# Kernel tuning notes

Measured on AMD Instinct MI355X. Metric: run time of the kernel, lower is better.

## Reference

```python
import jax, jax.numpy as jnp
import numpy as np

D = 768        # TEXT_DIM
N = 50         # seq len (h,w = 1,50 in source)
HEADS = 8
LABEL_SIZE = 50
B = 512
EPS_COS = 1e-8
EPS_LN = 1e-5


def _egce(x, w):
    # EGCE source not provided in repo snippet; implemented as ECA-style efficient
    # gated channel excitation: GAP over HW -> 1D conv (k=3) over channels -> sigmoid gate.
    gap = x.mean(axis=(2, 3))                      # [b, c]
    p = jnp.pad(gap, ((0, 0), (1, 1)))
    att = jax.nn.sigmoid(w[0] * p[:, :-2] + w[1] * p[:, 1:-1] + w[2] * p[:, 2:])
    return x * att[:, :, None, None]


def _lstm(x, Wih, Whh, bih, bhh):
    # PyTorch single-layer batch_first LSTM, gate order i,f,g,o, zero init state.
    b, n, d = x.shape
    xg = jnp.einsum('bnd,gd->bng', x, Wih) + bih + bhh   # [b, n, 4d]
    def step(carry, xt):
        h, c = carry
        g = xt + h @ Whh.T
        i, f, gg, o = jnp.split(g, 4, axis=-1)
        c = jax.nn.sigmoid(f) * c + jax.nn.sigmoid(i) * jnp.tanh(gg)
        h = jax.nn.sigmoid(o) * jnp.tanh(c)
        return (h, c), h
    h0 = jnp.zeros((b, d), x.dtype)
    _, ys = jax.lax.scan(step, (h0, h0), jnp.swapaxes(xg, 0, 1))
    return jnp.swapaxes(ys, 0, 1)


def _cross_attn(q_in, kv_in, qW, qb, kW, kb, vW, vb):
    b, n, d = q_in.shape
    dh = d // HEADS
    q = (q_in @ qW.T + qb).reshape(b, n, HEADS, dh).transpose(0, 2, 1, 3)
    k = (kv_in @ kW.T + kb).reshape(b, -1, HEADS, dh).transpose(0, 2, 1, 3)
    v = (kv_in @ vW.T + vb).reshape(b, -1, HEADS, dh).transpose(0, 2, 1, 3)
    attn = jax.nn.softmax(jnp.einsum('bhqd,bhkd->bhqk', q, k) * dh ** -0.5, axis=-1)
    # NOTE: faithful to source: einsum('bhqk,bhvd->bhqd') sums k and v INDEPENDENTLY
    out = jnp.einsum('bhqk,bhvd->bhqd', attn, v)
    return out.transpose(0, 2, 1, 3).reshape(b, n, d)


def _ln(x, g, b):
    m = x.mean(-1, keepdims=True)
    v = ((x - m) ** 2).mean(-1, keepdims=True)
    return (x - m) * jax.lax.rsqrt(v + EPS_LN) * g + b


def setup_inputs() -> dict:
    key = jax.random.key(0)
    ks = jax.random.split(key, 24)
    s = 0.02
    def w(k, shape):
        return jax.random.normal(k, shape, jnp.float32) * s
    vis_emb = w(ks[0], (LABEL_SIZE + 1, D)).at[LABEL_SIZE].set(0.0)
    ac_emb = w(ks[1], (LABEL_SIZE + 1, D)).at[LABEL_SIZE].set(0.0)
    inp = {
        'text_embedding': jax.random.normal(ks[2], (B, N, D), jnp.float32),
        'visual_ids': jax.random.randint(ks[3], (B, N), 0, LABEL_SIZE),
        'acoustic_ids': jax.random.randint(ks[4], (B, N), 0, LABEL_SIZE),
        'vis_emb': vis_emb,
        'ac_emb': ac_emb,
        'egce_w': w(ks[5], (3,)) + 0.3,
        'lstm_Wih': w(ks[6], (4 * D, D)),
        'lstm_Whh': w(ks[7], (4 * D, D)),
        'lstm_bih': jnp.zeros((4 * D,), jnp.float32),
        'lstm_bhh': jnp.zeros((4 * D,), jnp.float32),
        'ln_g': jnp.ones((D,), jnp.float32),
        'ln_b': jnp.zeros((D,), jnp.float32),
        'concat_W': w(ks[8], (D, 3 * D)),
        'concat_b': jnp.zeros((D,), jnp.float32),
        'hybrid_W': w(ks[9], (D, 3 * D)),
        'hybrid_b': jnp.zeros((D,), jnp.float32),
        # stacked cross-attention params, index 0 = cross_att_t, 1 = cross_att_a, 2 = cross_att_v
        'ca_qW': w(ks[10], (3, D, D)), 'ca_qb': w(ks[11], (3, D)),
        'ca_kW': w(ks[12], (3, D, D)), 'ca_kb': w(ks[13], (3, D)),
        'ca_vW': w(ks[14], (3, D, D)), 'ca_vb': w(ks[15], (3, D)),
    }
    return inp


def _forward(text_embedding, vis_emb, ac_emb, egce_w, lstm_Wih, lstm_Whh,
             lstm_bih, lstm_bhh, ln_g, ln_b, concat_W, concat_b, hybrid_W,
             hybrid_b, ca_qW, ca_qb, ca_kW, ca_kb, ca_vW, ca_vb,
             visual_ids, acoustic_ids):
    b, n, c = text_embedding.shape
    visual_ = jax.nn.relu(vis_emb[visual_ids])
    acoustic_ = ac_emb[acoustic_ids]
    # faithful reshape (NOT transpose) [b,n,c] -> [b,c,1,n] -> egce -> [b,n,c]
    text = _egce(text_embedding.reshape(b, c, 1, n), egce_w).reshape(b, n, c)
    visual_ = _egce(visual_.reshape(b, c, 1, n), egce_w).reshape(b, n, c)
    acoustic_ = _egce(acoustic_.reshape(b, c, 1, n), egce_w).reshape(b, n, c)

    # ---- AFI (vectorized over batch via masks instead of Python loop) ----
    def cos(x, y):
        xm, ym = x.mean(1), y.mean(1)
        nx = jnp.maximum(jnp.sqrt((xm * xm).sum(-1)), EPS_COS)
        ny = jnp.maximum(jnp.sqrt((ym * ym).sum(-1)), EPS_COS)
        return (xm * ym).sum(-1) / (nx * ny)
    rtv, rta, rva = cos(text, visual_), cos(text, acoustic_), cos(visual_, acoustic_)
    delta = (rtv + rta + rva) / 3.0
    joint = (rtv + rta + rva) / 3.0   # identical to delta in source
    cat = jnp.concatenate([text, visual_, acoustic_], axis=-1)  # [b,n,3d]
    f_concat = cat @ concat_W.T + concat_b
    f_hybrid = cat @ hybrid_W.T + hybrid_b
    tv = _cross_attn(text, visual_, ca_qW[0], ca_qb[0], ca_kW[0], ca_kb[0], ca_vW[0], ca_vb[0])
    ta = _cross_attn(text, acoustic_, ca_qW[1], ca_qb[1], ca_kW[1], ca_kb[1], ca_vW[1], ca_vb[1])
    va = _cross_attn(visual_, acoustic_, ca_qW[2], ca_qb[2], ca_kW[2], ca_kb[2], ca_vW[2], ca_vb[2])
    f_cross = (tv + ta + va) / 3.0
    m1 = ((rtv > delta) & (rta > delta) & (rva > delta))[:, None, None]
    m2 = (joint > delta)[:, None, None]
    fusion = jnp.where(m1, f_concat, jnp.where(m2, f_hybrid, f_cross))
    # dropout is identity in eval mode

    shift = _ln(fusion + text, ln_g, ln_b)
    out = _lstm(shift, lstm_Wih, lstm_Whh, lstm_bih, lstm_bhh) + text
    return out


def reference(text_embedding, visual_ids, acoustic_ids, vis_emb, ac_emb, egce_w,
              lstm_Wih, lstm_Whh, lstm_bih, lstm_bhh, ln_g, ln_b, concat_W,
              concat_b, hybrid_W, hybrid_b, ca_qW, ca_qb, ca_kW, ca_kb, ca_vW, ca_vb):
    return _forward(text_embedding, vis_emb, ac_emb, egce_w, lstm_Wih, lstm_Whh,
                    lstm_bih, lstm_bhh, ln_g, ln_b, concat_W, concat_b, hybrid_W,
                    hybrid_b, ca_qW, ca_qb, ca_kW, ca_kb, ca_vW, ca_vb,
                    visual_ids, acoustic_ids)
```

## Files before the change

kernel.cpp:

```cpp
#include <hip/hip_runtime.h>
#include <hip/hip_bf16.h>
#include <math.h>

#define B 512
#define N 50
#define D 768
#define G4 3072
#define KCAT 1536
#define BN (B*N)
#define FLAT (N*D)
#define KC 1536
#define CCH 6400

typedef __hip_bfloat16 bf16;
typedef short short8 __attribute__((ext_vector_type(8)));
typedef float floatx4 __attribute__((ext_vector_type(4)));

__device__ __forceinline__ float sigf(float x){ return 1.0f/(1.0f+expf(-x)); }
__device__ __forceinline__ float u2f(unsigned short u){ return __uint_as_float(((unsigned int)u)<<16); }
__device__ __forceinline__ unsigned short f2u(float f){ bf16 h=__float2bfloat16(f); return *(unsigned short*)&h; }

__global__ __launch_bounds__(256) void egce_fused(
    const float* __restrict__ text, const int* __restrict__ vid, const int* __restrict__ aid,
    const float* __restrict__ vemb, const float* __restrict__ aemb, const float* __restrict__ egw,
    float* __restrict__ att_t, unsigned short* __restrict__ catAB){
  __shared__ float buf[CCH];
  __shared__ float gt[D+2], gv[D+2], ga[D+2];
  __shared__ float attvS[D], attaS[D];
  __shared__ int vidS[N], aidS[N];
  int b=blockIdx.x, tid=threadIdx.x;
  if(tid<N){ vidS[tid]=vid[b*N+tid]; aidS[tid]=aid[b*N+tid]; }
  if(tid==0){ gt[0]=gv[0]=ga[0]=0.f; gt[D+1]=gv[D+1]=ga[D+1]=0.f; }
  __syncthreads();
  const float* tb = text + (size_t)b*FLAT;
  for(int c=0;c<6;c++){
    int j0=c*CCH;
    for(int it=0;it<25;it++) buf[it*256+tid]=tb[j0+it*256+tid];
    __syncthreads();
    if(tid<128){ float s=0.f; for(int p=0;p<50;p++) s+=buf[tid*50+p]; gt[c*128+tid+1]=s*(1.f/50.f); }
    __syncthreads();
    for(int it=0;it<25;it++){ int j=j0+it*256+tid; int n=j/D, d=j-n*D;
      float v=vemb[vidS[n]*D+d]; buf[it*256+tid]=v>0.f?v:0.f; }
    __syncthreads();
    if(tid<128){ float s=0.f; for(int p=0;p<50;p++) s+=buf[tid*50+p]; gv[c*128+tid+1]=s*(1.f/50.f); }
    __syncthreads();
    for(int it=0;it<25;it++){ int j=j0+it*256+tid; int n=j/D, d=j-n*D;
      buf[it*256+tid]=aemb[aidS[n]*D+d]; }
    __syncthreads();
    if(tid<128){ float s=0.f; for(int p=0;p<50;p++) s+=buf[tid*50+p]; ga[c*128+tid+1]=s*(1.f/50.f); }
    __syncthreads();
  }
  float w0=egw[0],w1=egw[1],w2=egw[2];
  for(int ch=tid;ch<D;ch+=256){
    att_t[(size_t)b*D+ch]=sigf(w0*gt[ch]+w1*gt[ch+1]+w2*gt[ch+2]);
    attvS[ch]=sigf(w0*gv[ch]+w1*gv[ch+1]+w2*gv[ch+2]);
    attaS[ch]=sigf(w0*ga[ch]+w1*ga[ch+1]+w2*ga[ch+2]);
  }
  __syncthreads();
  float va[3]={0,0,0}, aa[3]={0,0,0};
  for(int n=0;n<N;n++){
    int idv=vidS[n], ida=aidS[n];
    #pragma unroll
    for(int q=0;q<3;q++){
      int d=q*256+tid;
      int ch=(n*D+d)/50;
      float vv=vemb[idv*D+d]; vv=vv>0.f?vv:0.f;
      va[q]+=vv*attvS[ch];
      aa[q]+=aemb[ida*D+d]*attaS[ch];
    }
  }
  for(int q=0;q<3;q++){
    int d=q*256+tid;
    catAB[(size_t)b*KC+d]    =f2u(va[q]);
    catAB[(size_t)b*KC+D+d]  =f2u(aa[q]);
  }
}

__global__ __launch_bounds__(256) void prep_weights(
    const float* __restrict__ Wih, const float* __restrict__ Whh,
    const float* __restrict__ bih, const float* __restrict__ bhh,
    unsigned short* __restrict__ Wcat, float* __restrict__ bsum){
  int np = blockIdx.x;
  int dg = np>>2, g = np&3;
  size_t src = (size_t)(g*D+dg)*D;
  for(int k=threadIdx.x;k<D;k+=256){
    Wcat[(size_t)np*KCAT + k]     = f2u(Whh[src+k]);
    Wcat[(size_t)np*KCAT + D + k] = f2u(Wih[src+k]);
  }
  if(threadIdx.x==0) bsum[np] = bih[g*D+dg] + bhh[g*D+dg];
}

__global__ __launch_bounds__(256) void prep_fcross(
    const float* __restrict__ vW, const float* __restrict__ vb,
    unsigned short* __restrict__ WcB, float* __restrict__ fb){
  int n = blockIdx.x;
  const float* W0 = vW; const float* W1 = vW + D*D; const float* W2 = vW + 2*D*D;
  for(int k=threadIdx.x;k<D;k+=256){
    WcB[(size_t)n*KC + k]     = f2u(W0[(size_t)n*D+k]);
    WcB[(size_t)n*KC + D + k] = f2u(W1[(size_t)n*D+k] + W2[(size_t)n*D+k]);
  }
  if(threadIdx.x==0) fb[n] = 50.f*(vb[n]+vb[D+n]+vb[2*D+n]);
}

__global__ __launch_bounds__(256) void fcross_mfma(
    const unsigned short* __restrict__ catAB, const unsigned short* __restrict__ WcB,
    const float* __restrict__ fb, float* __restrict__ fcross){
  __shared__ unsigned short Ash[32*40];
  __shared__ unsigned short Bsh[64*40];
  int tid=threadIdx.x;
  int bx=blockIdx.x, by=blockIdx.y;
  int lane=tid&63, w=tid>>6;
  int l15=lane&15, lq=lane>>4;
  int arow=tid>>3, aseg=(tid&7)*4;
  int brow=tid>>2, bseg=(tid&3)*8;
  floatx4 acc0={},acc1={};
  const unsigned short* aG = catAB + (size_t)(by*32 + arow)*KC + aseg;
  const unsigned short* bG = WcB   + (size_t)(bx*64 + brow)*KC + bseg;
  for(int k0=0;k0<KC;k0+=32){
    *(uint2*)&Ash[arow*40 + aseg] = *(const uint2*)(aG + k0);
    *(uint4*)&Bsh[brow*40 + bseg] = *(const uint4*)(bG + k0);
    __syncthreads();
    short8 a0=*(const short8*)&Ash[l15*40 + lq*8];
    short8 a1=*(const short8*)&Ash[(16+l15)*40 + lq*8];
    short8 bb=*(const short8*)&Bsh[(w*16 + l15)*40 + lq*8];
    acc0=__builtin_amdgcn_mfma_f32_16x16x32_bf16(a0,bb,acc0,0,0,0);
    acc1=__builtin_amdgcn_mfma_f32_16x16x32_bf16(a1,bb,acc1,0,0,0);
    __syncthreads();
  }
  int n = bx*64 + w*16 + l15;
  float bias = fb[n];
  #pragma unroll
  for(int r=0;r<4;r++){
    int m0 = by*32 + lq*4 + r;
    fcross[(size_t)m0*D + n]      = (acc0[r] + bias)*(1.f/3.f);
    fcross[(size_t)(m0+16)*D + n] = (acc1[r] + bias)*(1.f/3.f);
  }
}

__global__ __launch_bounds__(256) void fuse_ln(
    const float* __restrict__ text, const float* __restrict__ att_t,
    const float* __restrict__ fcross, const float* __restrict__ lng,
    const float* __restrict__ lnb, bf16* __restrict__ shift){
  int row = blockIdx.x;
  int b = row/N, n = row - b*N;
  int tid=threadIdx.x;
  float v[3];
  for(int q=0;q<3;q++){
    int d=q*256+tid;
    int ch=(n*D+d)/50;
    v[q] = text[(size_t)row*D+d]*att_t[(size_t)b*D+ch] + fcross[(size_t)b*D+d];
  }
  __shared__ float red[256];
  red[tid]=v[0]+v[1]+v[2]; __syncthreads();
  for(int st=128;st>0;st>>=1){ if(tid<st) red[tid]+=red[tid+st]; __syncthreads(); }
  float m = red[0]*(1.f/768.f);
  __syncthreads();
  float s2=0.f;
  for(int q=0;q<3;q++){ float dl=v[q]-m; s2+=dl*dl; }
  red[tid]=s2; __syncthreads();
  for(int st=128;st>0;st>>=1){ if(tid<st) red[tid]+=red[tid+st]; __syncthreads(); }
  float var = red[0]*(1.f/768.f);
  float rs = 1.f/sqrtf(var+1e-5f);
  for(int q=0;q<3;q++){
    int d=q*256+tid;
    shift[(size_t)row*D+d]=__float2bfloat16((v[q]-m)*rs*lng[d]+lnb[d]);
  }
}

__global__ __launch_bounds__(256) void lstm_fused(
    const unsigned short* __restrict__ shift, const unsigned short* __restrict__ Wcat,
    const float* __restrict__ bsum, const unsigned short* __restrict__ hprev,
    unsigned short* __restrict__ hnext, float* __restrict__ cbuf,
    const float* __restrict__ text, const float* __restrict__ att_t,
    float* __restrict__ out, int t){
  __shared__ unsigned short Ab[2][64*40];
  __shared__ unsigned short Bb[2][128*40];
  const int tid=threadIdx.x;
  const int id = blockIdx.x;
  const int xcd = id & 7;
  const int j = id >> 3;
  const int bx = xcd*6 + (j>>4);
  const int by = j & 15;
  const int lane=tid&63, w=tid>>6, l15=lane&15, lq=lane>>4;

  const int sra = tid>>2, ca=(tid&3)*8;
  const int arow = sra&31, ah = sra>>5;
  const int dA = sra*40 + ca;
  const int b_a = by*32 + arow;
  const unsigned short* hThr = hprev + (size_t)b_a*D + ah*32 + ca;
  const unsigned short* xThr = shift + ((size_t)b_a*N + t)*D + ah*32 + ca;

  const int sr0 = tid>>2,        c0=(tid&3)*8;
  const int sr1 = (tid+256)>>2,  c1=(tid&3)*8;
  const int br0 = sr0&63, bh0 = sr0>>6;
  const int br1 = sr1&63, bh1 = sr1>>6;
  const unsigned short* bThr0 = Wcat + (size_t)(bx*64+br0)*KCAT + bh0*32 + c0;
  const unsigned short* bThr1 = Wcat + (size_t)(bx*64+br1)*KCAT + bh1*32 + c1;
  const int dB0 = sr0*40 + c0, dB1 = sr1*40 + c1;

  const int kbase  = t ? 0 : 768;
  const int nIters = t ? 24 : 12;

  floatx4 acc0={}, acc1={};

  {
    const unsigned short* ap = (kbase<768) ? (hThr + kbase) : (xThr + (kbase-768));
    uint4 pA  = *(const uint4*)ap;
    uint4 pB0 = *(const uint4*)(bThr0 + kbase);
    uint4 pB1 = *(const uint4*)(bThr1 + kbase);
    *(uint4*)&Ab[0][dA]  = pA;
    *(uint4*)&Bb[0][dB0] = pB0;
    *(uint4*)&Bb[0][dB1] = pB1;
  }
  __syncthreads();

  #pragma unroll 2
  for(int it=0; it<nIters; ++it){
    const int cur = it&1;
    uint4 nA, nB0, nB1;
    const bool more = (it+1 < nIters);
    if(more){
      int kg = kbase + (it+1)*64;
      const unsigned short* ap = (kg<768) ? (hThr + kg) : (xThr + (kg-768));
      nA  = *(const uint4*)ap;
      nB0 = *(const uint4*)(bThr0 + kg);
      nB1 = *(const uint4*)(bThr1 + kg);
    }
    short8 Wf0 = *(const short8*)&Bb[cur][(w*16+l15)*40 + lq*8];
    short8 Wf1 = *(const short8*)&Bb[cur][(64 + w*16+l15)*40 + lq*8];
    short8 X00 = *(const short8*)&Ab[cur][(l15)*40 + lq*8];
    short8 X10 = *(const short8*)&Ab[cur][(16+l15)*40 + lq*8];
    short8 X01 = *(const short8*)&Ab[cur][(32+l15)*40 + lq*8];
    short8 X11 = *(const short8*)&Ab[cur][(48+l15)*40 + lq*8];
    acc0 = __builtin_amdgcn_mfma_f32_16x16x32_bf16(Wf0, X00, acc0, 0,0,0);
    acc1 = __builtin_amdgcn_mfma_f32_16x16x32_bf16(Wf0, X10, acc1, 0,0,0);
    acc0 = __builtin_amdgcn_mfma_f32_16x16x32_bf16(Wf1, X01, acc0, 0,0,0);
    acc1 = __builtin_amdgcn_mfma_f32_16x16x32_bf16(Wf1, X11, acc1, 0,0,0);
    if(more){
      *(uint4*)&Ab[cur^1][dA]  = nA;
      *(uint4*)&Bb[cur^1][dB0] = nB0;
      *(uint4*)&Bb[cur^1][dB1] = nB1;
    }
    __syncthreads();
  }

  const int nb = bx*64 + w*16 + lq*4;
  const int dg = nb>>2;
  floatx4 bs = *(const floatx4*)&bsum[nb];
  #pragma unroll
  for(int mf=0; mf<2; ++mf){
    floatx4 a = mf ? acc1 : acc0;
    int b = by*32 + mf*16 + l15;
    float gi=a[0]+bs[0], gf=a[1]+bs[1], gg=a[2]+bs[2], go=a[3]+bs[3];
    float co = t ? cbuf[(size_t)b*D+dg] : 0.f;
    float cn = sigf(gf)*co + sigf(gi)*tanhf(gg);
    float hn = sigf(go)*tanhf(cn);
    cbuf[(size_t)b*D+dg] = cn;
    hnext[(size_t)b*D+dg] = f2u(hn);
    int ch = (t*D+dg)/50;
    size_t oi = ((size_t)b*N + t)*D + dg;
    out[oi] = hn + text[oi]*att_t[(size_t)b*D+ch];
  }
}

extern "C" void kernel_launch(void* const* d_in, const int* in_sizes, int n_in,
                              void* d_out, int out_size, void* d_ws, size_t ws_size,
                              hipStream_t stream){
  const float* text=(const float*)d_in[0];
  const int*  vid =(const int*) d_in[1];
  const int*  aid =(const int*) d_in[2];
  const float* vemb=(const float*)d_in[3];
  const float* aemb=(const float*)d_in[4];
  const float* egw =(const float*)d_in[5];
  const float* Wih =(const float*)d_in[6];
  const float* Whh =(const float*)d_in[7];
  const float* bih =(const float*)d_in[8];
  const float* bhh =(const float*)d_in[9];
  const float* lng =(const float*)d_in[10];
  const float* lnb =(const float*)d_in[11];
  const float* vW  =(const float*)d_in[20];
  const float* vb  =(const float*)d_in[21];
  float* out = (float*)d_out;

  float* W = (float*)d_ws;
  const size_t S = (size_t)B*D;
  float* att_t = W;
  float* fcross= att_t + S;
  float* cbuf  = fcross + S;
  float* bsum  = cbuf + S;
  float* fb    = bsum + G4;
  unsigned short* Wcat = (unsigned short*)(fb + D);
  unsigned short* WcB  = Wcat + (size_t)G4*KCAT;
  unsigned short* catAB= WcB + (size_t)D*KC;
  unsigned short* hA0  = catAB + (size_t)B*KC;
  unsigned short* hA1  = hA0 + S;
  bf16*  shift = (bf16*)(hA1 + S);

  prep_weights<<<G4,256,0,stream>>>(Wih,Whh,bih,bhh,Wcat,bsum);
  prep_fcross<<<D,256,0,stream>>>(vW,vb,WcB,fb);
  egce_fused<<<B,256,0,stream>>>(text,vid,aid,vemb,aemb,egw,att_t,catAB);
  fcross_mfma<<<dim3(12,16),256,0,stream>>>(catAB,WcB,fb,fcross);
  fuse_ln<<<BN,256,0,stream>>>(text,att_t,fcross,lng,lnb,shift);

  for(int t=0;t<N;t++){
    unsigned short* hp = (t&1)? hA1 : hA0;
    unsigned short* hn = (t&1)? hA0 : hA1;
    lstm_fused<<<768,256,0,stream>>>((const unsigned short*)shift,Wcat,bsum,
                                     hp,hn,cbuf,text,att_t,out,t);
  }
}
```

Measured before the change: 1.237 ms.

## Triple-buffer LSTM GEMM LDS pipeline and vectorize EGCE gather loads

The LSTM step kernel moves from double to triple LDS buffering, keeping global prefetches two iterations ahead so global latency can overlap two MFMA iterations instead of one. The EGCE kernel switches its text and embedding loads to float4 and computes the gated pooling with 192 threads, each handling four channels. The extra buffer raises LDS use per block, and the stores now happen before the MFMA reads, which changes ordering and could cost occupancy.

Result: no change. 1.234 ms (-0.2%).

```diff
diff --git a/kernel.cpp b/kernel.cpp
--- a/kernel.cpp
+++ b/kernel.cpp
@@ -32,20 +32,26 @@
   if(tid<N){ vidS[tid]=vid[b*N+tid]; aidS[tid]=aid[b*N+tid]; }
   if(tid==0){ gt[0]=gv[0]=ga[0]=0.f; gt[D+1]=gv[D+1]=ga[D+1]=0.f; }
   __syncthreads();
-  const float* tb = text + (size_t)b*FLAT;
+  const float4* tb4 = (const float4*)(text + (size_t)b*FLAT);
   for(int c=0;c<6;c++){
     int j0=c*CCH;
-    for(int it=0;it<25;it++) buf[it*256+tid]=tb[j0+it*256+tid];
+    for(int i=tid;i<1600;i+=256) ((float4*)buf)[i] = tb4[c*1600+i];
     __syncthreads();
     if(tid<128){ float s=0.f; for(int p=0;p<50;p++) s+=buf[tid*50+p]; gt[c*128+tid+1]=s*(1.f/50.f); }
     __syncthreads();
-    for(int it=0;it<25;it++){ int j=j0+it*256+tid; int n=j/D, d=j-n*D;
-      float v=vemb[vidS[n]*D+d]; buf[it*256+tid]=v>0.f?v:0.f; }
+    for(int i=tid;i<1600;i+=256){
+      int j=j0+i*4; int n=j/D, d=j-n*D;
+      float4 v=*(const float4*)&vemb[(size_t)vidS[n]*D+d];
+      v.x=fmaxf(v.x,0.f); v.y=fmaxf(v.y,0.f); v.z=fmaxf(v.z,0.f); v.w=fmaxf(v.w,0.f);
+      ((float4*)buf)[i]=v;
+    }
     __syncthreads();
     if(tid<128){ float s=0.f; for(int p=0;p<50;p++) s+=buf[tid*50+p]; gv[c*128+tid+1]=s*(1.f/50.f); }
     __syncthreads();
-    for(int it=0;it<25;it++){ int j=j0+it*256+tid; int n=j/D, d=j-n*D;
-      buf[it*256+tid]=aemb[aidS[n]*D+d]; }
+    for(int i=tid;i<1600;i+=256){
+      int j=j0+i*4; int n=j/D, d=j-n*D;
+      ((float4*)buf)[i]=*(const float4*)&aemb[(size_t)aidS[n]*D+d];
+    }
     __syncthreads();
     if(tid<128){ float s=0.f; for(int p=0;p<50;p++) s+=buf[tid*50+p]; ga[c*128+tid+1]=s*(1.f/50.f); }
     __syncthreads();
@@ -57,22 +63,22 @@
     attaS[ch]=sigf(w0*ga[ch]+w1*ga[ch+1]+w2*ga[ch+2]);
   }
   __syncthreads();
-  float va[3]={0,0,0}, aa[3]={0,0,0};
-  for(int n=0;n<N;n++){
-    int idv=vidS[n], ida=aidS[n];
-    #pragma unroll
-    for(int q=0;q<3;q++){
-      int d=q*256+tid;
-      int ch=(n*D+d)/50;
-      float vv=vemb[idv*D+d]; vv=vv>0.f?vv:0.f;
-      va[q]+=vv*attvS[ch];
-      aa[q]+=aemb[ida*D+d]*attaS[ch];
-    }
-  }
-  for(int q=0;q<3;q++){
-    int d=q*256+tid;
-    catAB[(size_t)b*KC+d]    =f2u(va[q]);
-    catAB[(size_t)b*KC+D+d]  =f2u(aa[q]);
+  if(tid<192){
+    float vax=0,vay=0,vaz=0,vaw=0, aax=0,aay=0,aaz=0,aaw=0;
+    int d0=tid*4;
+    for(int n=0;n<N;n++){
+      int idv=vidS[n], ida=aidS[n];
+      float4 v=*(const float4*)&vemb[(size_t)idv*D+d0];
+      float4 a=*(const float4*)&aemb[(size_t)ida*D+d0];
+      int base=n*D+d0;
+      int c0=base/50, c1=(base+1)/50, c2=(base+2)/50, c3=(base+3)/50;
+      vax+=fmaxf(v.x,0.f)*attvS[c0]; vay+=fmaxf(v.y,0.f)*attvS[c1];
+      vaz+=fmaxf(v.z,0.f)*attvS[c2]; vaw+=fmaxf(v.w,0.f)*attvS[c3];
+      aax+=a.x*attaS[c0]; aay+=a.y*attaS[c1]; aaz+=a.z*attaS[c2]; aaw+=a.w*attaS[c3];
+    }
+    unsigned short* cb=&catAB[(size_t)b*KC];
+    cb[d0]=f2u(vax); cb[d0+1]=f2u(vay); cb[d0+2]=f2u(vaz); cb[d0+3]=f2u(vaw);
+    cb[D+d0]=f2u(aax); cb[D+d0+1]=f2u(aay); cb[D+d0+2]=f2u(aaz); cb[D+d0+3]=f2u(aaw);
   }
 }
 
@@ -173,8 +179,8 @@
     unsigned short* __restrict__ hnext, float* __restrict__ cbuf,
     const float* __restrict__ text, const float* __restrict__ att_t,
     float* __restrict__ out, int t){
-  __shared__ unsigned short Ab[2][64*40];
-  __shared__ unsigned short Bb[2][128*40];
+  __shared__ unsigned short Ab[3][64*40];
+  __shared__ unsigned short Bb[3][128*40];
   const int tid=threadIdx.x;
   const int id = blockIdx.x;
   const int xcd = id & 7;
@@ -202,29 +208,40 @@
   const int nIters = t ? 24 : 12;
 
   floatx4 acc0={}, acc1={};
+  uint4 rA, rB0, rB1;
 
   {
     const unsigned short* ap = (kbase<768) ? (hThr + kbase) : (xThr + (kbase-768));
-    uint4 pA  = *(const uint4*)ap;
-    uint4 pB0 = *(const uint4*)(bThr0 + kbase);
-    uint4 pB1 = *(const uint4*)(bThr1 + kbase);
-    *(uint4*)&Ab[0][dA]  = pA;
-    *(uint4*)&Bb[0][dB0] = pB0;
-    *(uint4*)&Bb[0][dB1] = pB1;
+    rA  = *(const uint4*)ap;
+    rB0 = *(const uint4*)(bThr0 + kbase);
+    rB1 = *(const uint4*)(bThr1 + kbase);
+    *(uint4*)&Ab[0][dA]  = rA;
+    *(uint4*)&Bb[0][dB0] = rB0;
+    *(uint4*)&Bb[0][dB1] = rB1;
+  }
+  {
+    int kg = kbase + 64;
+    const unsigned short* ap = (kg<768) ? (hThr + kg) : (xThr + (kg-768));
+    rA  = *(const uint4*)ap;
+    rB0 = *(const uint4*)(bThr0 + kg);
+    rB1 = *(const uint4*)(bThr1 + kg);
   }
   __syncthreads();
 
-  #pragma unroll 2
+  int cur=0, nxt=1, thr=2;
+  #pragma unroll 3
   for(int it=0; it<nIters; ++it){
-    const int cur = it&1;
-    uint4 nA, nB0, nB1;
-    const bool more = (it+1 < nIters);
-    if(more){
-      int kg = kbase + (it+1)*64;
+    if(it+1 < nIters){
+      *(uint4*)&Ab[nxt][dA]  = rA;
+      *(uint4*)&Bb[nxt][dB0] = rB0;
+      *(uint4*)&Bb[nxt][dB1] = rB1;
+    }
+    if(it+2 < nIters){
+      int kg = kbase + (it+2)*64;
       const unsigned short* ap = (kg<768) ? (hThr + kg) : (xThr + (kg-768));
-      nA  = *(const uint4*)ap;
-      nB0 = *(const uint4*)(bThr0 + kg);
-      nB1 = *(const uint4*)(bThr1 + kg);
+      rA  = *(const uint4*)ap;
+      rB0 = *(const uint4*)(bThr0 + kg);
+      rB1 = *(const uint4*)(bThr1 + kg);
     }
     short8 Wf0 = *(const short8*)&Bb[cur][(w*16+l15)*40 + lq*8];
     short8 Wf1 = *(const short8*)&Bb[cur][(64 + w*16+l15)*40 + lq*8];
@@ -236,12 +253,8 @@
     acc1 = __builtin_amdgcn_mfma_f32_16x16x32_bf16(Wf0, X10, acc1, 0,0,0);
     acc0 = __builtin_amdgcn_mfma_f32_16x16x32_bf16(Wf1, X01, acc0, 0,0,0);
     acc1 = __builtin_amdgcn_mfma_f32_16x16x32_bf16(Wf1, X11, acc1, 0,0,0);
-    if(more){
-      *(uint4*)&Ab[cur^1][dA]  = nA;
-      *(uint4*)&Bb[cur^1][dB0] = nB0;
-      *(uint4*)&Bb[cur^1][dB1] = nB1;
-    }
-    __syncthreads();
+    __syncthreads();
+    int tmp=cur; cur=nxt; nxt=thr; thr=tmp;
   }
 
   const int nb = bx*64 + w*16 + lq*4;
```
